# Optimization experiments

Measured on AMD Instinct MI355X. Metric: run time of the kernel, lower is better.

## Reference

```python
import jax, jax.numpy as jnp
import numpy as np

ATT = 64   # attention_size (becomes number of split chunks / effective heads)
NH = 16    # num_heads (becomes chunk width / effective head dim)


def setup_inputs() -> dict:
    key = jax.random.key(0)
    ks = jax.random.split(key, 9)
    B, T, E = 4, 1024, 1024
    AH = ATT * NH  # 1024
    s = 0.02
    return {
        "x": jax.random.normal(ks[0], (B, T, E), jnp.float32),
        "Wq": jax.random.normal(ks[1], (E, AH), jnp.float32) * s,
        "bq": jax.random.normal(ks[2], (AH,), jnp.float32) * s,
        "Wk": jax.random.normal(ks[3], (E, AH), jnp.float32) * s,
        "bk": jax.random.normal(ks[4], (AH,), jnp.float32) * s,
        "Wv": jax.random.normal(ks[5], (E, AH), jnp.float32) * s,
        "bv": jax.random.normal(ks[6], (AH,), jnp.float32) * s,
        "Wo": jax.random.normal(ks[7], (AH, E), jnp.float32) * s,
        "bo": jax.random.normal(ks[8], (E,), jnp.float32) * s,
    }


def reference(x, Wq, bq, Wk, bk, Wv, bv, Wo, bo):
    B, T, E = x.shape
    A, H = ATT, NH

    q = x @ Wq + bq  # [B,T,A*H]
    k = x @ Wk + bk
    v = x @ Wv + bv

    # torch.split(m, num_heads, dim=2) -> A chunks of width H; cat along dim 0
    def split_cat(m):
        # [B,T,A,H] -> [A,B,T,H] -> [A*B,T,H]
        return m.reshape(B, T, A, H).transpose(2, 0, 1, 3).reshape(A * B, T, H)

    q = split_cat(q)
    k = split_cat(k)
    v = split_cat(v)

    scores = jnp.einsum('bqh,bkh->bqk', q, k) / (A ** 0.5)  # [A*B,T,T]
    attn = jax.nn.softmax(scores, axis=-1)
    z = jnp.einsum('bqk,bkh->bqh', attn, v)  # [A*B,T,H]

    # faithful to torch: contiguous [A*B,T,H] viewed as [B, T, A*H] (no un-permute)
    z = z.reshape(B, T, A * H)
    return z @ Wo + bo
```

## Files before the change

kernel.cpp:

```cpp
#include <hip/hip_runtime.h>
#include <hip/hip_bf16.h>


typedef __bf16 bf16_t;
typedef bf16_t bf16x8 __attribute__((ext_vector_type(8)));
typedef short  s16x4 __attribute__((ext_vector_type(4)));
typedef float  f32x4 __attribute__((ext_vector_type(4)));

#define SCALE_LOG2E 0.18033688011112042f

__device__ __forceinline__ void async16(const bf16_t* g, void* l) {
    __builtin_amdgcn_global_load_lds(
        (const __attribute__((address_space(1))) unsigned int*)g,
        (__attribute__((address_space(3))) unsigned int*)l,
        16, 0, 0);
}

__global__ __launch_bounds__(256) void cast_f32_bf16(
    const float* __restrict__ in, bf16_t* __restrict__ out, int n8)
{
    int i = blockIdx.x * 256 + threadIdx.x;
    if (i >= n8) return;
    const float4* p = (const float4*)in + (size_t)i * 2;
    float4 a = p[0], b = p[1];
    bf16x8 o;
    o[0] = (bf16_t)a.x; o[1] = (bf16_t)a.y; o[2] = (bf16_t)a.z; o[3] = (bf16_t)a.w;
    o[4] = (bf16_t)b.x; o[5] = (bf16_t)b.y; o[6] = (bf16_t)b.z; o[7] = (bf16_t)b.w;
    *((bf16x8*)out + i) = o;
}

__global__ __launch_bounds__(256) void transpose_cast(
    const float* __restrict__ W0, const float* __restrict__ W1,
    const float* __restrict__ W2, const float* __restrict__ W3,
    bf16_t* __restrict__ out)
{
    __shared__ float st[32][33];
    const float* W = (blockIdx.z == 0) ? W0 : (blockIdx.z == 1) ? W1
                   : (blockIdx.z == 2) ? W2 : W3;
    bf16_t* o = out + (size_t)blockIdx.z * 1024 * 1024;
    const int n0 = blockIdx.x * 32, k0 = blockIdx.y * 32;
    const int t = threadIdx.x;
    const int r = t >> 3, c4 = (t & 7) * 4;
    float4 v = *(const float4*)(W + (size_t)(k0 + r) * 1024 + n0 + c4);
    st[r][c4 + 0] = v.x; st[r][c4 + 1] = v.y; st[r][c4 + 2] = v.z; st[r][c4 + 3] = v.w;
    __syncthreads();
    bf16_t tmp[4] __attribute__((aligned(8)));
    #pragma unroll
    for (int i = 0; i < 4; ++i) tmp[i] = (bf16_t)st[c4 + i][r];
    *(uint2*)(o + (size_t)(n0 + r) * 1024 + k0 + c4) = *(const uint2*)tmp;
}

template<bool FUSED, int MT>
__global__ __launch_bounds__(256, 3) void gemm_glds(
    const bf16_t* __restrict__ A, const bf16_t* __restrict__ Bt,
    const float* __restrict__ b0, const float* __restrict__ b1,
    const float* __restrict__ b2,
    bf16_t* __restrict__ Qo, bf16_t* __restrict__ Ko, bf16_t* __restrict__ Vo,
    float* __restrict__ Fo)
{
    const int K = 1024;
    __shared__ __align__(16) bf16_t As[MT * 32];
    __shared__ __align__(16) bf16_t Bs[128 * 32];

    constexpr int NTPW = (MT == 128) ? 4 : 2;
    constexpr int JA   = MT / 64;

    const int tid  = threadIdx.x;
    const int wave = tid >> 6;
    const int lane = tid & 63;
    const int quad = lane >> 4;
    const int l16  = lane & 15;
    const int m0 = blockIdx.y * MT;
    const int n0 = blockIdx.x * 128;
    const int wm = (MT == 128) ? (wave >> 1) * 64 : 0;
    const int wn = (MT == 128) ? (wave & 1) * 64 : wave * 32;

    int goffA[JA], goffB[2];
    #pragma unroll
    for (int j = 0; j < JA; ++j) {
        const int row = j * 64 + (tid >> 2);
        const int cl  = (tid & 3) ^ ((row >> 1) & 3);
        goffA[j] = (m0 + row) * K + cl * 8;
    }
    #pragma unroll
    for (int j = 0; j < 2; ++j) {
        const int row = j * 64 + (tid >> 2);
        const int cl  = (tid & 3) ^ ((row >> 1) & 3);
        goffB[j] = (n0 + row) * K + cl * 8;
    }
    const int ldsoff = wave * 1024;

    f32x4 acc[4][NTPW] = {};
    const int sw = (l16 >> 1) & 3;

    for (int k0 = 0; k0 < K; k0 += 32) {
        #pragma unroll
        for (int j = 0; j < JA; ++j)
            async16(A + goffA[j] + k0, (char*)As + j * 4096 + ldsoff);
        #pragma unroll
        for (int j = 0; j < 2; ++j)
            async16(Bt + goffB[j] + k0, (char*)Bs + j * 4096 + ldsoff);
        __syncthreads();

        bf16x8 af[4], bfr[NTPW];
        #pragma unroll
        for (int mt = 0; mt < 4; ++mt)
            af[mt] = *(const bf16x8*)(&As[(wm + mt * 16 + l16) * 32 + (quad ^ sw) * 8]);
        #pragma unroll
        for (int nt = 0; nt < NTPW; ++nt)
            bfr[nt] = *(const bf16x8*)(&Bs[(wn + nt * 16 + l16) * 32 + (quad ^ sw) * 8]);
        #pragma unroll
        for (int mt = 0; mt < 4; ++mt)
            #pragma unroll
            for (int nt = 0; nt < NTPW; ++nt)
                acc[mt][nt] = __builtin_amdgcn_mfma_f32_16x16x32_bf16(
                    af[mt], bfr[nt], acc[mt][nt], 0, 0, 0);
        __syncthreads();
    }

    if (FUSED) {
        const int sel = n0 >> 10;
        const float* bias = (sel == 0) ? b0 : (sel == 1) ? b1 : b2;
        bf16_t* Cout      = (sel == 0) ? Qo : (sel == 1) ? Ko : Vo;
        const float scl   = (sel == 1) ? SCALE_LOG2E : 1.0f;
        const int nb = n0 & 1023;
        #pragma unroll
        for (int nt = 0; nt < NTPW; ++nt) {
            const int n = nb + wn + nt * 16 + l16;
            const float bb = bias[n];
            #pragma unroll
            for (int mt = 0; mt < 4; ++mt)
                #pragma unroll
                for (int i = 0; i < 4; ++i) {
                    const int m = m0 + wm + mt * 16 + quad * 4 + i;
                    Cout[(size_t)m * 1024 + n] = (bf16_t)((acc[mt][nt][i] + bb) * scl);
                }
        }
    } else {
        #pragma unroll
        for (int nt = 0; nt < NTPW; ++nt) {
            const int n = n0 + wn + nt * 16 + l16;
            const float bb = b0[n];
            #pragma unroll
            for (int mt = 0; mt < 4; ++mt)
                #pragma unroll
                for (int i = 0; i < 4; ++i) {
                    const int m = m0 + wm + mt * 16 + quad * 4 + i;
                    Fo[(size_t)m * 1024 + n] = acc[mt][nt][i] + bb;
                }
        }
    }
}

__global__ __launch_bounds__(256, 4) void attn_kernel(
    const bf16_t* __restrict__ Q, const bf16_t* __restrict__ K,
    const bf16_t* __restrict__ V, bf16_t* __restrict__ Z)
{
    __shared__ __align__(16) bf16_t Vt[2][16 * 72];

    const int tid  = threadIdx.x;
    const int wave = tid >> 6;
    const int lane = tid & 63;
    const int quad = lane >> 4;
    const int l16  = lane & 15;
    const int hd = blockIdx.x >> 2;
    const int qc = blockIdx.x & 3;
    const int a = hd >> 2, b = hd & 3;
    const int col0 = a * 16;
    const int qbase = qc * 256 + wave * 64;

    bf16x8 qf[4] = {};
    if (quad < 2) {
        #pragma unroll
        for (int qs = 0; qs < 4; ++qs)
            qf[qs] = *(const bf16x8*)(Q +
                (size_t)(b * 1024 + qbase + qs * 16 + l16) * 1024 + col0 + quad * 8);
    }

    const bf16_t* Kp = K + (size_t)(b * 1024 + l16) * 1024 + col0 + quad * 8;
    bf16x8 kf[2][4] = {};
    if (quad < 2) {
        #pragma unroll
        for (int kt = 0; kt < 4; ++kt)
            kf[0][kt] = *(const bf16x8*)(Kp + (size_t)(kt * 16) * 1024);
    }

    const int r  = tid >> 2;
    const int dq = (tid & 3) * 4;
    const bf16_t* Vp = V + (size_t)(b * 1024 + r) * 1024 + col0 + dq;

    uint2 vv = *(const uint2*)Vp;
    {
        bf16_t t4[4] __attribute__((aligned(8)));
        *(uint2*)t4 = vv;
        #pragma unroll
        for (int ii = 0; ii < 4; ++ii)
            Vt[0][(dq + ii) * 72 + r] = t4[ii];
    }
    vv = *(const uint2*)(Vp + (size_t)64 * 1024);
    __syncthreads();

    const s16x4 ones = { 0x3F80, 0x3F80, 0x3F80, 0x3F80 };

    f32x4 zacc[4] = {};
    f32x4 lacc[4] = {};

    #pragma unroll
    for (int j = 0; j < 16; ++j) {
        const int cur = j & 1, nxt = cur ^ 1;

        if (j < 15 && quad < 2) {
            #pragma unroll
            for (int kt = 0; kt < 4; ++kt)
                kf[nxt][kt] = *(const bf16x8*)(Kp + (size_t)((j + 1) * 64 + kt * 16) * 1024);
        }
        if (j < 15) {
            bf16_t t4[4] __attribute__((aligned(8)));
            *(uint2*)t4 = vv;
            #pragma unroll
            for (int ii = 0; ii < 4; ++ii)
                Vt[nxt][(dq + ii) * 72 + r] = t4[ii];
            if (j < 14)
                vv = *(const uint2*)(Vp + (size_t)((j + 2) * 64) * 1024);
        }

        #pragma unroll
        for (int kt = 0; kt < 4; ++kt) {
            const s16x4 vfrag = __builtin_bit_cast(s16x4,
                *(const uint2*)(&Vt[cur][l16 * 72 + kt * 16 + quad * 4]));
            #pragma unroll
            for (int qs = 0; qs < 4; ++qs) {
                f32x4 zc = {0.f, 0.f, 0.f, 0.f};
                f32x4 s = __builtin_amdgcn_mfma_f32_16x16x32_bf16(
                    kf[cur][kt], qf[qs], zc, 0, 0, 0);
                unsigned int u0 = __builtin_bit_cast(unsigned int,
                    __builtin_amdgcn_exp2f(s[0])) + 0x8000u;
                unsigned int u1 = __builtin_bit_cast(unsigned int,
                    __builtin_amdgcn_exp2f(s[1])) + 0x8000u;
                unsigned int u2 = __builtin_bit_cast(unsigned int,
                    __builtin_amdgcn_exp2f(s[2])) + 0x8000u;
                unsigned int u3 = __builtin_bit_cast(unsigned int,
                    __builtin_amdgcn_exp2f(s[3])) + 0x8000u;
                uint2 w;
                w.x = __builtin_amdgcn_perm(u1, u0, 0x07060302u);
                w.y = __builtin_amdgcn_perm(u3, u2, 0x07060302u);
                const s16x4 pfrag = __builtin_bit_cast(s16x4, w);
                zacc[qs] = __builtin_amdgcn_mfma_f32_16x16x16bf16_1k(
                    vfrag, pfrag, zacc[qs], 0, 0, 0);
                lacc[qs] = __builtin_amdgcn_mfma_f32_16x16x16bf16_1k(
                    ones, pfrag, lacc[qs], 0, 0, 0);
            }
        }
        __syncthreads();
    }

    #pragma unroll
    for (int qs = 0; qs < 4; ++qs) {
        const float inv = 1.0f / lacc[qs][0];
        const int q = qbase + qs * 16 + l16;
        bf16_t o4[4] __attribute__((aligned(8)));
        #pragma unroll
        for (int i = 0; i < 4; ++i) o4[i] = (bf16_t)(zacc[qs][i] * inv);
        *(uint2*)(Z + ((size_t)hd * 1024 + q) * 16 + quad * 4) = *(const uint2*)o4;
    }
}

extern "C" void kernel_launch(void* const* d_in, const int* in_sizes, int n_in,
                              void* d_out, int out_size, void* d_ws, size_t ws_size,
                              hipStream_t stream) {
    const float* x  = (const float*)d_in[0];
    const float* Wq = (const float*)d_in[1];
    const float* bq = (const float*)d_in[2];
    const float* Wk = (const float*)d_in[3];
    const float* bk = (const float*)d_in[4];
    const float* Wv = (const float*)d_in[5];
    const float* bv = (const float*)d_in[6];
    const float* Wo = (const float*)d_in[7];
    const float* bo = (const float*)d_in[8];
    float* out = (float*)d_out;

    char* ws = (char*)d_ws;
    bf16_t* x_bf = (bf16_t*)(ws);
    bf16_t* Wt   = (bf16_t*)(ws + (8u << 20));
    bf16_t* Qb   = (bf16_t*)(ws + (16u << 20));
    bf16_t* Kb   = (bf16_t*)(ws + (24u << 20));
    bf16_t* Vb   = (bf16_t*)(ws + (32u << 20));
    bf16_t* Zb   = (bf16_t*)(ws + (40u << 20));
    bf16_t* WtO  = Wt + (size_t)3 * 1024 * 1024;

    cast_f32_bf16<<<dim3(2048), dim3(256), 0, stream>>>(x, x_bf, 524288);
    transpose_cast<<<dim3(32, 32, 4), dim3(256), 0, stream>>>(Wq, Wk, Wv, Wo, Wt);

    gemm_glds<true, 128><<<dim3(24, 32), dim3(256), 0, stream>>>(
        x_bf, Wt, bq, bk, bv, Qb, Kb, Vb, nullptr);

    attn_kernel<<<dim3(1024), dim3(256), 0, stream>>>(Qb, Kb, Vb, Zb);

    gemm_glds<false, 64><<<dim3(8, 64), dim3(256), 0, stream>>>(
        Zb, WtO, bo, nullptr, nullptr, nullptr, nullptr, nullptr, out);
}
```

Before: 191.6 us.

## Stage full transposed V in LDS upfront and drop per-tile barriers

The attention kernel now loads the whole 1024-key V slice for its head into a transposed LDS buffer before the main loop, replacing the per-tile double-buffered V staging. This removes the 16 per-tile __syncthreads, leaving a single barrier. The main loop becomes an explicit two-tile ping-pong over K register buffers with unroll 1 to limit code size and register pressure. The cost is about 33 KB of LDS per block, which may reduce blocks per CU below the launch-bound target. The V load latency is also exposed up front instead of overlapped with compute.

```diff
diff --git a/kernel.cpp b/kernel.cpp
--- a/kernel.cpp
+++ b/kernel.cpp
@@ -156,7 +156,7 @@
     const bf16_t* __restrict__ Q, const bf16_t* __restrict__ K,
     const bf16_t* __restrict__ V, bf16_t* __restrict__ Z)
 {
-    __shared__ __align__(16) bf16_t Vt[2][16 * 72];
+    __shared__ __align__(16) bf16_t Vt[16][1032];
 
     const int tid  = threadIdx.x;
     const int wave = tid >> 6;
@@ -169,6 +169,19 @@
     const int col0 = a * 16;
     const int qbase = qc * 256 + wave * 64;
 
+    const int r  = tid >> 2;
+    const int dq = (tid & 3) * 4;
+    const bf16_t* Vp = V + (size_t)(b * 1024 + r) * 1024 + col0 + dq;
+    #pragma unroll 4
+    for (int t = 0; t < 16; ++t) {
+        uint2 vv = *(const uint2*)(Vp + (size_t)(t * 64) * 1024);
+        bf16_t t4[4] __attribute__((aligned(8)));
+        *(uint2*)t4 = vv;
+        #pragma unroll
+        for (int ii = 0; ii < 4; ++ii)
+            Vt[dq + ii][t * 64 + r] = t4[ii];
+    }
+
     bf16x8 qf[4] = {};
     if (quad < 2) {
         #pragma unroll
@@ -178,26 +191,13 @@
     }
 
     const bf16_t* Kp = K + (size_t)(b * 1024 + l16) * 1024 + col0 + quad * 8;
-    bf16x8 kf[2][4] = {};
+    bf16x8 kfA[4] = {}, kfB[4] = {};
     if (quad < 2) {
         #pragma unroll
         for (int kt = 0; kt < 4; ++kt)
-            kf[0][kt] = *(const bf16x8*)(Kp + (size_t)(kt * 16) * 1024);
-    }
-
-    const int r  = tid >> 2;
-    const int dq = (tid & 3) * 4;
-    const bf16_t* Vp = V + (size_t)(b * 1024 + r) * 1024 + col0 + dq;
-
-    uint2 vv = *(const uint2*)Vp;
-    {
-        bf16_t t4[4] __attribute__((aligned(8)));
-        *(uint2*)t4 = vv;
-        #pragma unroll
-        for (int ii = 0; ii < 4; ++ii)
-            Vt[0][(dq + ii) * 72 + r] = t4[ii];
-    }
-    vv = *(const uint2*)(Vp + (size_t)64 * 1024);
+            kfA[kt] = *(const bf16x8*)(Kp + (size_t)(kt * 16) * 1024);
+    }
+
     __syncthreads();
 
     const s16x4 ones = { 0x3F80, 0x3F80, 0x3F80, 0x3F80 };
@@ -205,54 +205,50 @@
     f32x4 zacc[4] = {};
     f32x4 lacc[4] = {};
 
-    #pragma unroll
-    for (int j = 0; j < 16; ++j) {
-        const int cur = j & 1, nxt = cur ^ 1;
-
-        if (j < 15 && quad < 2) {
-            #pragma unroll
-            for (int kt = 0; kt < 4; ++kt)
-                kf[nxt][kt] = *(const bf16x8*)(Kp + (size_t)((j + 1) * 64 + kt * 16) * 1024);
-        }
-        if (j < 15) {
-            bf16_t t4[4] __attribute__((aligned(8)));
-            *(uint2*)t4 = vv;
-            #pragma unroll
-            for (int ii = 0; ii < 4; ++ii)
-                Vt[nxt][(dq + ii) * 72 + r] = t4[ii];
-            if (j < 14)
-                vv = *(const uint2*)(Vp + (size_t)((j + 2) * 64) * 1024);
-        }
-
-        #pragma unroll
-        for (int kt = 0; kt < 4; ++kt) {
-            const s16x4 vfrag = __builtin_bit_cast(s16x4,
-                *(const uint2*)(&Vt[cur][l16 * 72 + kt * 16 + quad * 4]));
-            #pragma unroll
-            for (int qs = 0; qs < 4; ++qs) {
-                f32x4 zc = {0.f, 0.f, 0.f, 0.f};
-                f32x4 s = __builtin_amdgcn_mfma_f32_16x16x32_bf16(
-                    kf[cur][kt], qf[qs], zc, 0, 0, 0);
-                unsigned int u0 = __builtin_bit_cast(unsigned int,
-                    __builtin_amdgcn_exp2f(s[0])) + 0x8000u;
-                unsigned int u1 = __builtin_bit_cast(unsigned int,
-                    __builtin_amdgcn_exp2f(s[1])) + 0x8000u;
-                unsigned int u2 = __builtin_bit_cast(unsigned int,
-                    __builtin_amdgcn_exp2f(s[2])) + 0x8000u;
-                unsigned int u3 = __builtin_bit_cast(unsigned int,
-                    __builtin_amdgcn_exp2f(s[3])) + 0x8000u;
-                uint2 w;
-                w.x = __builtin_amdgcn_perm(u1, u0, 0x07060302u);
-                w.y = __builtin_amdgcn_perm(u3, u2, 0x07060302u);
-                const s16x4 pfrag = __builtin_bit_cast(s16x4, w);
-                zacc[qs] = __builtin_amdgcn_mfma_f32_16x16x16bf16_1k(
-                    vfrag, pfrag, zacc[qs], 0, 0, 0);
-                lacc[qs] = __builtin_amdgcn_mfma_f32_16x16x16bf16_1k(
-                    ones, pfrag, lacc[qs], 0, 0, 0);
-            }
-        }
-        __syncthreads();
-    }
+#define ATTN_TILE(JIDX, KFCUR, KFNXT, DO_PREFETCH)                            \
+    {                                                                         \
+        const int j_ = (JIDX);                                                \
+        if (DO_PREFETCH && quad < 2) {                                        \
+            _Pragma("unroll")                                                 \
+            for (int kt = 0; kt < 4; ++kt)                                    \
+                KFNXT[kt] = *(const bf16x8*)(                                 \
+                    Kp + (size_t)((j_ + 1) * 64 + kt * 16) * 1024);           \
+        }                                                                     \
+        _Pragma("unroll")                                                     \
+        for (int kt = 0; kt < 4; ++kt) {                                      \
+            const s16x4 vfrag = __builtin_bit_cast(s16x4,                     \
+                *(const uint2*)(&Vt[l16][j_ * 64 + kt * 16 + quad * 4]));     \
+            _Pragma("unroll")                                                 \
+            for (int qs = 0; qs < 4; ++qs) {                                  \
+                f32x4 zc = {0.f, 0.f, 0.f, 0.f};                              \
+                f32x4 s = __builtin_amdgcn_mfma_f32_16x16x32_bf16(            \
+                    KFCUR[kt], qf[qs], zc, 0, 0, 0);                          \
+                unsigned int u0 = __builtin_bit_cast(unsigned int,            \
+                    __builtin_amdgcn_exp2f(s[0])) + 0x8000u;                  \
+                unsigned int u1 = __builtin_bit_cast(unsigned int,            \
+                    __builtin_amdgcn_exp2f(s[1])) + 0x8000u;                  \
+                unsigned int u2 = __builtin_bit_cast(unsigned int,            \
+                    __builtin_amdgcn_exp2f(s[2])) + 0x8000u;                  \
+                unsigned int u3 = __builtin_bit_cast(unsigned int,            \
+                    __builtin_amdgcn_exp2f(s[3])) + 0x8000u;                  \
+                uint2 w;                                                      \
+                w.x = __builtin_amdgcn_perm(u1, u0, 0x07060302u);             \
+                w.y = __builtin_amdgcn_perm(u3, u2, 0x07060302u);             \
+                const s16x4 pfrag = __builtin_bit_cast(s16x4, w);             \
+                zacc[qs] = __builtin_amdgcn_mfma_f32_16x16x16bf16_1k(         \
+                    vfrag, pfrag, zacc[qs], 0, 0, 0);                         \
+                lacc[qs] = __builtin_amdgcn_mfma_f32_16x16x16bf16_1k(         \
+                    ones, pfrag, lacc[qs], 0, 0, 0);                          \
+            }                                                                 \
+        }                                                                     \
+    }
+
+    #pragma unroll 1
+    for (int j2 = 0; j2 < 8; ++j2) {
+        ATTN_TILE(2 * j2,     kfA, kfB, true)
+        ATTN_TILE(2 * j2 + 1, kfB, kfA, (j2 < 7))
+    }
+#undef ATTN_TILE
 
     #pragma unroll
     for (int qs = 0; qs < 4; ++qs) {
```

After: 192.2 us. About the same (+0.3%).
